# Optimization experiments

Hardware: AMD Instinct MI355X
Metric: run time of the kernel (lower is better)

Reference implementation:

```python
import jax, jax.numpy as jnp
import numpy as np

H = 128
EPS = 1e-5

def _layernorm(x, g, b):
    mu = jnp.mean(x, axis=-1, keepdims=True)
    var = jnp.mean(jnp.square(x - mu), axis=-1, keepdims=True)
    return (x - mu) * jax.lax.rsqrt(var + EPS) * g + b

def _block(x, W, b, g, be):
    # Linear -> LayerNorm -> ReLU (dropout is identity at eval)
    return jax.nn.relu(_layernorm(x @ W + b, g, be))

def setup_inputs() -> dict:
    key = jax.random.key(0)
    ks = jax.random.split(key, 12)
    B, N, C = 32, 4096, 512
    s1 = 1.0 / np.sqrt(H)
    s2 = 1.0 / np.sqrt(2 * H)
    return {
        "fine_features": jax.random.normal(ks[0], (B, N, H), jnp.float32),
        "coarse_features": jax.random.normal(ks[1], (B, C, H), jnp.float32),
        "global_features": jax.random.normal(ks[2], (B, N, H), jnp.float32),
        "atom_to_coarse": jax.random.randint(ks[3], (B, N), 0, 600),  # some >= C (invalid)
        "W_pool": jax.random.uniform(ks[4], (H, H), jnp.float32, -s1, s1),
        "b_pool": jnp.zeros((H,), jnp.float32),
        "g_pool": jnp.ones((H,), jnp.float32),
        "be_pool": jnp.zeros((H,), jnp.float32),
        "W_unpool": jax.random.uniform(ks[5], (H, H), jnp.float32, -s1, s1),
        "b_unpool": jnp.zeros((H,), jnp.float32),
        "g_unpool": jnp.ones((H,), jnp.float32),
        "be_unpool": jnp.zeros((H,), jnp.float32),
        "W_gate": jax.random.uniform(ks[6], (2 * H, H), jnp.float32, -s2, s2),
        "b_gate": jnp.zeros((H,), jnp.float32),
        "W_glob": jax.random.uniform(ks[7], (2 * H, H), jnp.float32, -s2, s2),
        "b_glob": jnp.zeros((H,), jnp.float32),
        "g_glob": jnp.ones((H,), jnp.float32),
        "be_glob": jnp.zeros((H,), jnp.float32),
    }

def reference(fine_features, coarse_features, global_features, atom_to_coarse,
              W_pool, b_pool, g_pool, be_pool,
              W_unpool, b_unpool, g_unpool, be_unpool,
              W_gate, b_gate, W_glob, b_glob, g_glob, be_glob):
    B, N, Hd = fine_features.shape
    C = coarse_features.shape[1]
    idx = atom_to_coarse
    valid = (idx >= 0) & (idx < C)                      # [B,N]

    # ---- batched scatter-add pooling via flat segment_sum ----
    # invalid atoms routed to extra bucket C per batch element
    seg = jnp.where(valid, idx, C) + jnp.arange(B, dtype=idx.dtype)[:, None] * (C + 1)
    pooled = jax.ops.segment_sum(fine_features.reshape(B * N, Hd),
                                 seg.reshape(-1), num_segments=B * (C + 1))
    pooled = pooled.reshape(B, C + 1, Hd)[:, :C]        # [B,C,H]
    counts = jax.ops.segment_sum(valid.reshape(-1).astype(jnp.float32),
                                 seg.reshape(-1), num_segments=B * (C + 1))
    counts = counts.reshape(B, C + 1)[:, :C]
    coarse_from_fine = pooled / jnp.maximum(counts, 1.0)[..., None]
    coarse_from_fine = _block(coarse_from_fine, W_pool, b_pool, g_pool, be_pool)

    # ---- gather unpooling ----
    safe = jnp.where(valid, idx, 0)
    gathered = jnp.take_along_axis(coarse_features, safe[:, :, None], axis=1)  # [B,N,H]
    fine_from_coarse = jnp.where(valid[..., None], gathered, 0.0)
    fine_from_coarse = _block(fine_from_coarse, W_unpool, b_unpool, g_unpool, be_unpool)

    # ---- gated fusion ----
    fine_gate = jax.nn.sigmoid(jnp.concatenate([fine_features, fine_from_coarse], -1) @ W_gate + b_gate)
    fine_updated = fine_gate * fine_features + (1.0 - fine_gate) * fine_from_coarse
    coarse_gate = jax.nn.sigmoid(jnp.concatenate([coarse_features, coarse_from_fine], -1) @ W_gate + b_gate)
    coarse_updated = coarse_gate * coarse_features + (1.0 - coarse_gate) * coarse_from_fine

    # ---- global injection ----
    fine_wg = _block(jnp.concatenate([fine_updated, global_features], -1), W_glob, b_glob, g_glob, be_glob)
    fine_updated = fine_updated + 0.1 * fine_wg
    glob_c = jnp.broadcast_to(jnp.mean(global_features, axis=1, keepdims=True), (B, C, Hd))
    coarse_wg = _block(jnp.concatenate([coarse_updated, glob_c], -1), W_glob, b_glob, g_glob, be_glob)
    coarse_updated = coarse_updated + 0.1 * coarse_wg
    return (fine_updated, coarse_updated)
```

## Files before the change

### kernel.cpp

```cpp
#include <hip/hip_runtime.h>

typedef __bf16 bf16;
typedef bf16 bf16x8 __attribute__((ext_vector_type(8)));
typedef float f32x4 __attribute__((ext_vector_type(4)));

#define TPM 512
#define UPAD 136

#define NPOOL 1024
#define NGM   512
#define NPREP 64
#define NM1   128
#define NM0   1024

__device__ inline unsigned short f2bf(float f){
  union{ bf16 h; unsigned short u; } v; v.h = (bf16)f; return v.u;
}
__device__ inline float bf2f(unsigned short u){
  union{ unsigned short u; bf16 h; } v; v.u = u; return (float)v.h;
}
__device__ inline unsigned int pk2(float a, float b){
  return (unsigned int)f2bf(a) | ((unsigned int)f2bf(b) << 16);
}
union BF8 { bf16x8 v; unsigned int u[4]; };
__device__ inline bf16x8 pack8(float4 a, float4 b){
  BF8 r; r.u[0] = pk2(a.x, a.y); r.u[1] = pk2(a.z, a.w);
  r.u[2] = pk2(b.x, b.y); r.u[3] = pk2(b.z, b.w); return r.v;
}

__device__ inline void gll16(const unsigned short* g, unsigned short* l){
  __builtin_amdgcn_global_load_lds(
      (const __attribute__((address_space(1))) unsigned int*)g,
      (__attribute__((address_space(3))) unsigned int*)l, 16, 0, 0);
}
__device__ inline void stage_win(const unsigned short* __restrict__ src,
                                 unsigned short* half, int wave, int lane){
#pragma unroll
  for (int i = 0; i < 2; ++i){
    int slice = i*8 + wave;
    gll16(src + slice*512 + lane*8, half + slice*512 + lane*8);
  }
}

__device__ inline void gemm_win(const bf16x8 a[2], const unsigned short* half,
                                f32x4 acc[8], int lane){
#pragma unroll
  for (int kk = 0; kk < 2; ++kk){
    bf16x8 av = a[kk];
#pragma unroll
    for (int n = 0; n < 8; ++n){
      bf16x8 bv = *(const bf16x8*)(half + (size_t)((n*2 + kk)*512) + lane*8);
      acc[n] = __builtin_amdgcn_mfma_f32_16x16x32_bf16(av, bv, acc[n], 0, 0, 0);
    }
  }
}

__device__ inline void rowstats(const f32x4 acc[8], const float bia[8],
                                float mean[4], float rstd[4]){
#pragma unroll
  for (int ri = 0; ri < 4; ++ri){
    float s = 0.f, q = 0.f;
#pragma unroll
    for (int n = 0; n < 8; ++n){
      float z = acc[n][ri] + bia[n];
      s += z; q += z*z;
    }
#pragma unroll
    for (int m = 1; m < 16; m <<= 1){ s += __shfl_xor(s, m); q += __shfl_xor(q, m); }
    mean[ri] = s * (1.f/128.f);
    float var = q * (1.f/128.f) - mean[ri]*mean[ri];
    rstd[ri] = rsqrtf(var + 1e-5f);
  }
}

struct PoolSh {
  int sidx[4096];
  int rows[4096];
  int cnt[16], off[17], woff[16];
};
struct GmeanSh { float4 part4[16][32]; };
union PreSh { PoolSh p; GmeanSh g; };

__device__ void pool_body(PoolSh& sh, int pid,
                          const float* __restrict__ fine,
                          const int* __restrict__ idx,
                          unsigned short* __restrict__ pooled){
  int b = pid >> 5, g = pid & 31;
  int c0 = g * 16;
  int tid = threadIdx.x;
  const int* idx_b = idx + b*4096;
#pragma unroll
  for (int i = 0; i < 2; ++i)
    ((int4*)sh.sidx)[tid + i*TPM] = ((const int4*)idx_b)[tid + i*TPM];
  if (tid < 16) sh.cnt[tid] = 0;
  __syncthreads();
  for (int i = tid; i < 4096; i += TPM){
    unsigned d = (unsigned)(sh.sidx[i] - c0);
    if (d < 16u) atomicAdd(&sh.cnt[d], 1);
  }
  __syncthreads();
  if (tid == 0){
    int s = 0;
#pragma unroll
    for (int j = 0; j < 16; ++j){ sh.off[j] = s; s += sh.cnt[j]; }
    sh.off[16] = s;
  }
  __syncthreads();
  if (tid < 16) sh.woff[tid] = sh.off[tid];
  __syncthreads();
  for (int i = tid; i < 4096; i += TPM){
    unsigned d = (unsigned)(sh.sidx[i] - c0);
    if (d < 16u){ int p = atomicAdd(&sh.woff[d], 1); sh.rows[p] = i; }
  }
  __syncthreads();
  int hw = tid >> 5, l32 = tid & 31;
  const float* fb = fine + (size_t)b*4096*128;
  int o0 = sh.off[hw], o1 = sh.off[hw+1];
  float4 s = {0.f, 0.f, 0.f, 0.f};
  int m = o0;
  for (; m + 3 < o1; m += 4){
    float4 v0 = *((const float4*)(fb + (size_t)sh.rows[m+0]*128) + l32);
    float4 v1 = *((const float4*)(fb + (size_t)sh.rows[m+1]*128) + l32);
    float4 v2 = *((const float4*)(fb + (size_t)sh.rows[m+2]*128) + l32);
    float4 v3 = *((const float4*)(fb + (size_t)sh.rows[m+3]*128) + l32);
    s.x += (v0.x + v1.x) + (v2.x + v3.x);
    s.y += (v0.y + v1.y) + (v2.y + v3.y);
    s.z += (v0.z + v1.z) + (v2.z + v3.z);
    s.w += (v0.w + v1.w) + (v2.w + v3.w);
  }
  for (; m < o1; ++m){
    float4 v = *((const float4*)(fb + (size_t)sh.rows[m]*128) + l32);
    s.x += v.x; s.y += v.y; s.z += v.z; s.w += v.w;
  }
  float inv = 1.f / fmaxf((float)(o1 - o0), 1.f);
  unsigned short* po = pooled + ((size_t)(b*512 + c0 + hw))*128 + l32*4;
  uint2 w2; w2.x = pk2(s.x*inv, s.y*inv); w2.y = pk2(s.z*inv, s.w*inv);
  *(uint2*)po = w2;
}

__device__ void gmean_body(GmeanSh& sh, int gid,
                           const float* __restrict__ glob,
                           float* __restrict__ gmean){
  int b = gid >> 4, ch = gid & 15;
  int tid = threadIdx.x;
  int c4 = tid & 31, rg = tid >> 5;
  const float* gb = glob + ((size_t)b*4096 + ch*256)*128;
  float4 a = {0.f, 0.f, 0.f, 0.f};
#pragma unroll
  for (int i = 0; i < 16; ++i){
    int r = rg + i*16;
    float4 v = *(const float4*)(gb + (size_t)r*128 + c4*4);
    a.x += v.x; a.y += v.y; a.z += v.z; a.w += v.w;
  }
  sh.part4[rg][c4] = a;
  __syncthreads();
  if (tid < 32){
    float4 s = sh.part4[0][tid];
#pragma unroll
    for (int g = 1; g < 16; ++g){
      float4 v = sh.part4[g][tid];
      s.x += v.x; s.y += v.y; s.z += v.z; s.w += v.w;
    }
    float* gm = gmean + b*128 + tid*4;
    atomicAdd(&gm[0], s.x); atomicAdd(&gm[1], s.y);
    atomicAdd(&gm[2], s.z); atomicAdd(&gm[3], s.w);
  }
}

__device__ void prep_body(int e,
                          const float* __restrict__ Wp, const float* __restrict__ Wu,
                          const float* __restrict__ Wg, const float* __restrict__ Wgl,
                          unsigned short* __restrict__ WfP, unsigned short* __restrict__ WfU,
                          unsigned short* __restrict__ WfG, unsigned short* __restrict__ WfGl){
  int j = e & 7, lane = (e >> 3) & 63, frag = e >> 9;
  int kk = frag & 1, nblk = (frag >> 1) & 7, c = frag >> 4;
  int il = lane & 15, lg = lane >> 4;
  int col = nblk*16 + il;
  int k = c*64 + kk*32 + lg*8 + j;
  if (e < 16384){
    WfP[e] = f2bf(Wp[k*128 + col]);
    WfU[e] = f2bf(Wu[k*128 + col]);
  }
  WfG[e]  = f2bf(Wg[k*128 + col]);
  WfGl[e] = f2bf(Wgl[k*128 + col]);
}

__global__ __launch_bounds__(TPM) void k_pre(
    const float* __restrict__ fine, const int* __restrict__ idx,
    const float* __restrict__ glob,
    const float* __restrict__ Wp, const float* __restrict__ Wu,
    const float* __restrict__ Wg, const float* __restrict__ Wgl,
    unsigned short* __restrict__ pooled, float* __restrict__ gmean,
    unsigned short* __restrict__ WfP, unsigned short* __restrict__ WfU,
    unsigned short* __restrict__ WfG, unsigned short* __restrict__ WfGl){
  __shared__ __align__(16) PreSh sh;
  int bid = blockIdx.x;
  if (bid < NPOOL)             pool_body(sh.p, bid, fine, idx, pooled);
  else if (bid < NPOOL + NGM)  gmean_body(sh.g, bid - NPOOL, glob, gmean);
  else                         prep_body((bid - NPOOL - NGM)*TPM + threadIdx.x,
                                         Wp, Wu, Wg, Wgl, WfP, WfU, WfG, WfGl);
}

struct MegaSh {
  unsigned short wb[2][8192];
  unsigned short ubuf[8][16*UPAD];
};
template<int PATH>
__device__ void mega_body(MegaSh& sh, int bid,
    const float* __restrict__ a_src,
    const float* __restrict__ gath_src,
    const unsigned short* __restrict__ x1b,
    const int* __restrict__ idx,
    const float* __restrict__ gsrc,
    float gscale,
    const unsigned short* __restrict__ Wf1, const float* __restrict__ b1,
    const float* __restrict__ g1, const float* __restrict__ be1,
    const unsigned short* __restrict__ WfG, const float* __restrict__ bG,
    const unsigned short* __restrict__ WfGl, const float* __restrict__ bGl,
    const float* __restrict__ gGl, const float* __restrict__ beGl,
    float* __restrict__ out)
{
  int tid = threadIdx.x;
  int wave = tid >> 6, lane = tid & 63;
  int il = lane & 15, lg = lane >> 4;
  int row0 = bid * 128 + wave * 16;
  int b = (PATH == 0) ? (row0 >> 12) : (row0 >> 9);
  unsigned short* u = sh.ubuf[wave];

  stage_win(Wf1, sh.wb[0], wave, lane);
  bf16x8 a1[4];
  if (PATH == 0){
    int n0 = row0 & 4095;
    int ci = idx[b*4096 + n0 + il];
    bool valid = (unsigned)ci < 512u;
    const float* cr = gath_src + ((size_t)b*512 + (valid ? ci : 0))*128;
#pragma unroll
    for (int c = 0; c < 2; ++c)
#pragma unroll
      for (int kk = 0; kk < 2; ++kk){
        float4 f0 = {0.f,0.f,0.f,0.f}, f1 = {0.f,0.f,0.f,0.f};
        if (valid){
          f0 = *(const float4*)(cr + c*64 + kk*32 + lg*8);
          f1 = *(const float4*)(cr + c*64 + kk*32 + lg*8 + 4);
        }
        a1[c*2 + kk] = pack8(f0, f1);
      }
  } else {
    const unsigned short* pr = x1b + (size_t)(row0 + il)*128;
#pragma unroll
    for (int c = 0; c < 2; ++c)
#pragma unroll
      for (int kk = 0; kk < 2; ++kk)
        a1[c*2 + kk] = *(const bf16x8*)(pr + c*64 + kk*32 + lg*8);
  }
  __syncthreads();

  f32x4 acc[8] = {};
  bf16x8 af[2];
  float4 raw[8];
  const float* ar = a_src + (size_t)(row0 + il)*128;

  stage_win(Wf1 + 8192, sh.wb[1], wave, lane);
  af[0] = a1[0]; af[1] = a1[1];
  gemm_win(af, sh.wb[0], acc, lane);
  __syncthreads();

  stage_win(WfG, sh.wb[0], wave, lane);
  af[0] = a1[2]; af[1] = a1[3];
  gemm_win(af, sh.wb[1], acc, lane);
#pragma unroll
  for (int c = 0; c < 2; ++c)
#pragma unroll
    for (int kk = 0; kk < 2; ++kk){
      raw[(c*2+kk)*2+0] = *(const float4*)(ar + c*64 + kk*32 + lg*8);
      raw[(c*2+kk)*2+1] = *(const float4*)(ar + c*64 + kk*32 + lg*8 + 4);
    }
  {
    float bia[8], gmv[8], btv[8];
#pragma unroll
    for (int n = 0; n < 8; ++n){
      int col = n*16 + il;
      bia[n] = b1[col]; gmv[n] = g1[col]; btv[n] = be1[col];
    }
    float mean[4], rstd[4];
    rowstats(acc, bia, mean, rstd);
#pragma unroll
    for (int ri = 0; ri < 4; ++ri)
#pragma unroll
      for (int n = 0; n < 8; ++n){
        float z = acc[n][ri] + bia[n];
        float y = fmaxf((z - mean[ri])*rstd[ri]*gmv[n] + btv[n], 0.f);
        u[(lg*4 + ri)*UPAD + n*16 + il] = f2bf(y);
      }
  }
  __syncthreads();

  stage_win(WfG + 8192, sh.wb[1], wave, lane);
#pragma unroll
  for (int n = 0; n < 8; ++n) acc[n] = (f32x4){0.f,0.f,0.f,0.f};
  af[0] = pack8(raw[0], raw[1]); af[1] = pack8(raw[2], raw[3]);
  gemm_win(af, sh.wb[0], acc, lane);
  __syncthreads();

  stage_win(WfG + 16384, sh.wb[0], wave, lane);
  af[0] = pack8(raw[4], raw[5]); af[1] = pack8(raw[6], raw[7]);
  gemm_win(af, sh.wb[1], acc, lane);
  __syncthreads();

  stage_win(WfG + 24576, sh.wb[1], wave, lane);
  if (PATH == 0){
    const float* gr = gsrc + (size_t)(row0 + il)*128;
#pragma unroll
    for (int c = 0; c < 2; ++c)
#pragma unroll
      for (int kk = 0; kk < 2; ++kk){
        raw[(c*2+kk)*2+0] = *(const float4*)(gr + c*64 + kk*32 + lg*8);
        raw[(c*2+kk)*2+1] = *(const float4*)(gr + c*64 + kk*32 + lg*8 + 4);
      }
  } else {
    const float* gm = gsrc + b*128;
#pragma unroll
    for (int c = 0; c < 2; ++c)
#pragma unroll
      for (int kk = 0; kk < 2; ++kk){
        float4 f0 = *(const float4*)(gm + c*64 + kk*32 + lg*8);
        float4 f1 = *(const float4*)(gm + c*64 + kk*32 + lg*8 + 4);
        raw[(c*2+kk)*2+0] = (float4){f0.x*gscale, f0.y*gscale, f0.z*gscale, f0.w*gscale};
        raw[(c*2+kk)*2+1] = (float4){f1.x*gscale, f1.y*gscale, f1.z*gscale, f1.w*gscale};
      }
  }
  af[0] = *(const bf16x8*)(u + il*UPAD + 0*64 + 0*32 + lg*8);
  af[1] = *(const bf16x8*)(u + il*UPAD + 0*64 + 1*32 + lg*8);
  gemm_win(af, sh.wb[0], acc, lane);
  __syncthreads();

  stage_win(WfGl, sh.wb[0], wave, lane);
  af[0] = *(const bf16x8*)(u + il*UPAD + 1*64 + 0*32 + lg*8);
  af[1] = *(const bf16x8*)(u + il*UPAD + 1*64 + 1*32 + lg*8);
  gemm_win(af, sh.wb[1], acc, lane);
#pragma unroll
  for (int ri = 0; ri < 4; ++ri){
    int grow = (row0 + lg*4 + ri)*128;
#pragma unroll
    for (int n = 0; n < 8; ++n){
      int col = n*16 + il;
      float z = acc[n][ri] + bG[col];
      float gt = 1.f / (1.f + __expf(-z));
      float f  = a_src[(size_t)grow + col];
      int ua = (lg*4 + ri)*UPAD + col;
      float u1 = bf2f(u[ua]);
      u[ua] = f2bf(gt*f + (1.f - gt)*u1);
    }
  }
  __syncthreads();

  stage_win(WfGl + 8192, sh.wb[1], wave, lane);
#pragma unroll
  for (int n = 0; n < 8; ++n) acc[n] = (f32x4){0.f,0.f,0.f,0.f};
  af[0] = *(const bf16x8*)(u + il*UPAD + 0*64 + 0*32 + lg*8);
  af[1] = *(const bf16x8*)(u + il*UPAD + 0*64 + 1*32 + lg*8);
  gemm_win(af, sh.wb[0], acc, lane);
  __syncthreads();

  stage_win(WfGl + 16384, sh.wb[0], wave, lane);
  af[0] = *(const bf16x8*)(u + il*UPAD + 1*64 + 0*32 + lg*8);
  af[1] = *(const bf16x8*)(u + il*UPAD + 1*64 + 1*32 + lg*8);
  gemm_win(af, sh.wb[1], acc, lane);
  __syncthreads();

  stage_win(WfGl + 24576, sh.wb[1], wave, lane);
  af[0] = pack8(raw[0], raw[1]); af[1] = pack8(raw[2], raw[3]);
  gemm_win(af, sh.wb[0], acc, lane);
  __syncthreads();

  af[0] = pack8(raw[4], raw[5]); af[1] = pack8(raw[6], raw[7]);
  gemm_win(af, sh.wb[1], acc, lane);
  {
    float bia[8], gmv[8], btv[8];
#pragma unroll
    for (int n = 0; n < 8; ++n){
      int col = n*16 + il;
      bia[n] = bGl[col]; gmv[n] = gGl[col]; btv[n] = beGl[col];
    }
    float mean[4], rstd[4];
    rowstats(acc, bia, mean, rstd);
#pragma unroll
    for (int ri = 0; ri < 4; ++ri){
      int grow = (row0 + lg*4 + ri)*128;
#pragma unroll
      for (int n = 0; n < 8; ++n){
        int col = n*16 + il;
        float z = acc[n][ri] + bia[n];
        float y = fmaxf((z - mean[ri])*rstd[ri]*gmv[n] + btv[n], 0.f);
        float u2 = bf2f(u[(lg*4 + ri)*UPAD + col]);
        out[(size_t)grow + col] = u2 + 0.1f*y;
      }
    }
  }
}

__global__ __launch_bounds__(TPM, 4) void k_mega(
    const float* __restrict__ fine,
    const float* __restrict__ coarse,
    const int* __restrict__ idx,
    const float* __restrict__ glob,
    const unsigned short* __restrict__ pooled,
    const float* __restrict__ gmean,
    const unsigned short* __restrict__ WfP, const float* __restrict__ bP,
    const float* __restrict__ gP, const float* __restrict__ beP,
    const unsigned short* __restrict__ WfU, const float* __restrict__ bU,
    const float* __restrict__ gU, const float* __restrict__ beU,
    const unsigned short* __restrict__ WfG, const float* __restrict__ bG,
    const unsigned short* __restrict__ WfGl, const float* __restrict__ bGl,
    const float* __restrict__ gGl, const float* __restrict__ beGl,
    float* __restrict__ out_fine,
    float* __restrict__ out_coarse)
{
  __shared__ __align__(16) MegaSh sh;
  int bid = blockIdx.x;
  if (bid < NM1){
    mega_body<1>(sh, bid, coarse, nullptr, pooled, nullptr, gmean, 1.f/4096.f,
                 WfP, bP, gP, beP, WfG, bG, WfGl, bGl, gGl, beGl, out_coarse);
  } else {
    mega_body<0>(sh, bid - NM1, fine, coarse, nullptr, idx, glob, 1.0f,
                 WfU, bU, gU, beU, WfG, bG, WfGl, bGl, gGl, beGl, out_fine);
  }
}

extern "C" void kernel_launch(void* const* d_in, const int* in_sizes, int n_in,
                              void* d_out, int out_size, void* d_ws, size_t ws_size,
                              hipStream_t stream){
  const float* fine    = (const float*)d_in[0];
  const float* coarse  = (const float*)d_in[1];
  const float* glob    = (const float*)d_in[2];
  const int*   idx     = (const int*)  d_in[3];
  const float* W_pool  = (const float*)d_in[4];
  const float* b_pool  = (const float*)d_in[5];
  const float* g_pool  = (const float*)d_in[6];
  const float* be_pool = (const float*)d_in[7];
  const float* W_unpool  = (const float*)d_in[8];
  const float* b_unpool  = (const float*)d_in[9];
  const float* g_unpool  = (const float*)d_in[10];
  const float* be_unpool = (const float*)d_in[11];
  const float* W_gate = (const float*)d_in[12];
  const float* b_gate = (const float*)d_in[13];
  const float* W_glob = (const float*)d_in[14];
  const float* b_glob = (const float*)d_in[15];
  const float* g_glob = (const float*)d_in[16];
  const float* be_glob= (const float*)d_in[17];

  const int B = 32, N = 4096, C = 512;
  float* out_fine   = (float*)d_out;
  float* out_coarse = out_fine + (size_t)B*N*128;

  char* w = (char*)d_ws;
  unsigned short* WfP  = (unsigned short*)w; w += 16384*2;
  unsigned short* WfU  = (unsigned short*)w; w += 16384*2;
  unsigned short* WfG  = (unsigned short*)w; w += 32768*2;
  unsigned short* WfGl = (unsigned short*)w; w += 32768*2;
  float* gmean = (float*)w;                  w += B*128*4;
  unsigned short* pooled = (unsigned short*)w; w += (size_t)B*C*128*2;

  hipMemsetAsync(gmean, 0, B*128*4, stream);
  k_pre<<<NPOOL + NGM + NPREP, TPM, 0, stream>>>(
      fine, idx, glob, W_pool, W_unpool, W_gate, W_glob,
      pooled, gmean, WfP, WfU, WfG, WfGl);

  k_mega<<<NM1 + NM0, TPM, 0, stream>>>(
      fine, coarse, idx, glob, pooled, gmean,
      WfP, b_pool, g_pool, be_pool,
      WfU, b_unpool, g_unpool, be_unpool,
      WfG, b_gate, WfGl, b_glob, g_glob, be_glob,
      out_fine, out_coarse);
}
```

Measured before the change: 106.6 us.

## Halve mega-kernel block size and stream weights in finer 32-K double-buffered slices

Splits the mega kernel into 256-thread blocks covering 64 rows, doubling the grid, and separates the pool kernel's thread count from it. Weights are restaged in 8 KB slices, one per 32-wide K step, across a single 20-step double-buffered loop instead of 16 KB windows. The prep kernel's fragment layout is reordered to match. This halves LDS per block to allow more resident blocks and finer overlap of loads with MFMA, at the cost of more __syncthreads and weights being reloaded by twice as many blocks.

Result: slower. 262.9 us (+146.6%).

```diff
diff --git a/kernel.cpp b/kernel.cpp
--- a/kernel.cpp
+++ b/kernel.cpp
@@ -4,14 +4,15 @@
 typedef bf16 bf16x8 __attribute__((ext_vector_type(8)));
 typedef float f32x4 __attribute__((ext_vector_type(4)));
 
-#define TPM 512
+#define TPP 512
+#define TPM 256
 #define UPAD 136
 
 #define NPOOL 1024
 #define NGM   512
 #define NPREP 64
-#define NM1   128
-#define NM0   1024
+#define NM1   256
+#define NM0   2048
 
 __device__ inline unsigned short f2bf(float f){
   union{ bf16 h; unsigned short u; } v; v.h = (bf16)f; return v.u;
@@ -33,25 +34,18 @@
       (const __attribute__((address_space(1))) unsigned int*)g,
       (__attribute__((address_space(3))) unsigned int*)l, 16, 0, 0);
 }
-__device__ inline void stage_win(const unsigned short* __restrict__ src,
-                                 unsigned short* half, int wave, int lane){
-#pragma unroll
-  for (int i = 0; i < 2; ++i){
-    int slice = i*8 + wave;
-    gll16(src + slice*512 + lane*8, half + slice*512 + lane*8);
-  }
-}
-
-__device__ inline void gemm_win(const bf16x8 a[2], const unsigned short* half,
-                                f32x4 acc[8], int lane){
-#pragma unroll
-  for (int kk = 0; kk < 2; ++kk){
-    bf16x8 av = a[kk];
-#pragma unroll
-    for (int n = 0; n < 8; ++n){
-      bf16x8 bv = *(const bf16x8*)(half + (size_t)((n*2 + kk)*512) + lane*8);
-      acc[n] = __builtin_amdgcn_mfma_f32_16x16x32_bf16(av, bv, acc[n], 0, 0, 0);
-    }
+__device__ inline void stage8(const unsigned short* __restrict__ src,
+                              unsigned short* dst, int tid){
+  gll16(src + tid*8, dst + tid*8);
+  gll16(src + (tid + TPM)*8, dst + (tid + TPM)*8);
+}
+
+__device__ inline void gemm8(bf16x8 av, const unsigned short* wbuf,
+                             f32x4 acc[8], int lane){
+#pragma unroll
+  for (int n = 0; n < 8; ++n){
+    bf16x8 bv = *(const bf16x8*)(wbuf + n*512 + lane*8);
+    acc[n] = __builtin_amdgcn_mfma_f32_16x16x32_bf16(av, bv, acc[n], 0, 0, 0);
   }
 }
 
@@ -91,10 +85,10 @@
   const int* idx_b = idx + b*4096;
 #pragma unroll
   for (int i = 0; i < 2; ++i)
-    ((int4*)sh.sidx)[tid + i*TPM] = ((const int4*)idx_b)[tid + i*TPM];
+    ((int4*)sh.sidx)[tid + i*TPP] = ((const int4*)idx_b)[tid + i*TPP];
   if (tid < 16) sh.cnt[tid] = 0;
   __syncthreads();
-  for (int i = tid; i < 4096; i += TPM){
+  for (int i = tid; i < 4096; i += TPP){
     unsigned d = (unsigned)(sh.sidx[i] - c0);
     if (d < 16u) atomicAdd(&sh.cnt[d], 1);
   }
@@ -108,7 +102,7 @@
   __syncthreads();
   if (tid < 16) sh.woff[tid] = sh.off[tid];
   __syncthreads();
-  for (int i = tid; i < 4096; i += TPM){
+  for (int i = tid; i < 4096; i += TPP){
     unsigned d = (unsigned)(sh.sidx[i] - c0);
     if (d < 16u){ int p = atomicAdd(&sh.woff[d], 1); sh.rows[p] = i; }
   }
@@ -173,9 +167,10 @@
                           unsigned short* __restrict__ WfP, unsigned short* __restrict__ WfU,
                           unsigned short* __restrict__ WfG, unsigned short* __restrict__ WfGl){
   int j = e & 7, lane = (e >> 3) & 63, frag = e >> 9;
-  int kk = frag & 1, nblk = (frag >> 1) & 7, c = frag >> 4;
+  int n = frag & 7, kkc = frag >> 3;
+  int kk = kkc & 1, c = kkc >> 1;
   int il = lane & 15, lg = lane >> 4;
-  int col = nblk*16 + il;
+  int col = n*16 + il;
   int k = c*64 + kk*32 + lg*8 + j;
   if (e < 16384){
     WfP[e] = f2bf(Wp[k*128 + col]);
@@ -185,7 +180,7 @@
   WfGl[e] = f2bf(Wgl[k*128 + col]);
 }
 
-__global__ __launch_bounds__(TPM) void k_pre(
+__global__ __launch_bounds__(TPP) void k_pre(
     const float* __restrict__ fine, const int* __restrict__ idx,
     const float* __restrict__ glob,
     const float* __restrict__ Wp, const float* __restrict__ Wu,
@@ -197,13 +192,13 @@
   int bid = blockIdx.x;
   if (bid < NPOOL)             pool_body(sh.p, bid, fine, idx, pooled);
   else if (bid < NPOOL + NGM)  gmean_body(sh.g, bid - NPOOL, glob, gmean);
-  else                         prep_body((bid - NPOOL - NGM)*TPM + threadIdx.x,
+  else                         prep_body((bid - NPOOL - NGM)*TPP + threadIdx.x,
                                          Wp, Wu, Wg, Wgl, WfP, WfU, WfG, WfGl);
 }
 
 struct MegaSh {
-  unsigned short wb[2][8192];
-  unsigned short ubuf[8][16*UPAD];
+  unsigned short wb[2][4096];
+  unsigned short ubuf[4][16*UPAD];
 };
 template<int PATH>
 __device__ void mega_body(MegaSh& sh, int bid,
@@ -223,11 +218,11 @@
   int tid = threadIdx.x;
   int wave = tid >> 6, lane = tid & 63;
   int il = lane & 15, lg = lane >> 4;
-  int row0 = bid * 128 + wave * 16;
+  int row0 = bid * 64 + wave * 16;
   int b = (PATH == 0) ? (row0 >> 12) : (row0 >> 9);
   unsigned short* u = sh.ubuf[wave];
 
-  stage_win(Wf1, sh.wb[0], wave, lane);
+  stage8(Wf1, sh.wb[0], tid);
   bf16x8 a1[4];
   if (PATH == 0){
     int n0 = row0 & 4095;
@@ -256,146 +251,120 @@
   __syncthreads();
 
   f32x4 acc[8] = {};
-  bf16x8 af[2];
   float4 raw[8];
   const float* ar = a_src + (size_t)(row0 + il)*128;
 
-  stage_win(Wf1 + 8192, sh.wb[1], wave, lane);
-  af[0] = a1[0]; af[1] = a1[1];
-  gemm_win(af, sh.wb[0], acc, lane);
-  __syncthreads();
-
-  stage_win(WfG, sh.wb[0], wave, lane);
-  af[0] = a1[2]; af[1] = a1[3];
-  gemm_win(af, sh.wb[1], acc, lane);
-#pragma unroll
-  for (int c = 0; c < 2; ++c)
-#pragma unroll
-    for (int kk = 0; kk < 2; ++kk){
-      raw[(c*2+kk)*2+0] = *(const float4*)(ar + c*64 + kk*32 + lg*8);
-      raw[(c*2+kk)*2+1] = *(const float4*)(ar + c*64 + kk*32 + lg*8 + 4);
-    }
-  {
-    float bia[8], gmv[8], btv[8];
-#pragma unroll
-    for (int n = 0; n < 8; ++n){
-      int col = n*16 + il;
-      bia[n] = b1[col]; gmv[n] = g1[col]; btv[n] = be1[col];
-    }
-    float mean[4], rstd[4];
-    rowstats(acc, bia, mean, rstd);
-#pragma unroll
-    for (int ri = 0; ri < 4; ++ri)
-#pragma unroll
-      for (int n = 0; n < 8; ++n){
-        float z = acc[n][ri] + bia[n];
-        float y = fmaxf((z - mean[ri])*rstd[ri]*gmv[n] + btv[n], 0.f);
-        u[(lg*4 + ri)*UPAD + n*16 + il] = f2bf(y);
-      }
-  }
-  __syncthreads();
-
-  stage_win(WfG + 8192, sh.wb[1], wave, lane);
-#pragma unroll
-  for (int n = 0; n < 8; ++n) acc[n] = (f32x4){0.f,0.f,0.f,0.f};
-  af[0] = pack8(raw[0], raw[1]); af[1] = pack8(raw[2], raw[3]);
-  gemm_win(af, sh.wb[0], acc, lane);
-  __syncthreads();
-
-  stage_win(WfG + 16384, sh.wb[0], wave, lane);
-  af[0] = pack8(raw[4], raw[5]); af[1] = pack8(raw[6], raw[7]);
-  gemm_win(af, sh.wb[1], acc, lane);
-  __syncthreads();
-
-  stage_win(WfG + 24576, sh.wb[1], wave, lane);
-  if (PATH == 0){
-    const float* gr = gsrc + (size_t)(row0 + il)*128;
-#pragma unroll
-    for (int c = 0; c < 2; ++c)
-#pragma unroll
-      for (int kk = 0; kk < 2; ++kk){
-        raw[(c*2+kk)*2+0] = *(const float4*)(gr + c*64 + kk*32 + lg*8);
-        raw[(c*2+kk)*2+1] = *(const float4*)(gr + c*64 + kk*32 + lg*8 + 4);
-      }
-  } else {
-    const float* gm = gsrc + b*128;
-#pragma unroll
-    for (int c = 0; c < 2; ++c)
-#pragma unroll
-      for (int kk = 0; kk < 2; ++kk){
-        float4 f0 = *(const float4*)(gm + c*64 + kk*32 + lg*8);
-        float4 f1 = *(const float4*)(gm + c*64 + kk*32 + lg*8 + 4);
-        raw[(c*2+kk)*2+0] = (float4){f0.x*gscale, f0.y*gscale, f0.z*gscale, f0.w*gscale};
-        raw[(c*2+kk)*2+1] = (float4){f1.x*gscale, f1.y*gscale, f1.z*gscale, f1.w*gscale};
-      }
-  }
-  af[0] = *(const bf16x8*)(u + il*UPAD + 0*64 + 0*32 + lg*8);
-  af[1] = *(const bf16x8*)(u + il*UPAD + 0*64 + 1*32 + lg*8);
-  gemm_win(af, sh.wb[0], acc, lane);
-  __syncthreads();
-
-  stage_win(WfGl, sh.wb[0], wave, lane);
-  af[0] = *(const bf16x8*)(u + il*UPAD + 1*64 + 0*32 + lg*8);
-  af[1] = *(const bf16x8*)(u + il*UPAD + 1*64 + 1*32 + lg*8);
-  gemm_win(af, sh.wb[1], acc, lane);
-#pragma unroll
-  for (int ri = 0; ri < 4; ++ri){
-    int grow = (row0 + lg*4 + ri)*128;
-#pragma unroll
-    for (int n = 0; n < 8; ++n){
-      int col = n*16 + il;
-      float z = acc[n][ri] + bG[col];
-      float gt = 1.f / (1.f + __expf(-z));
-      float f  = a_src[(size_t)grow + col];
-      int ua = (lg*4 + ri)*UPAD + col;
-      float u1 = bf2f(u[ua]);
-      u[ua] = f2bf(gt*f + (1.f - gt)*u1);
-    }
-  }
-  __syncthreads();
-
-  stage_win(WfGl + 8192, sh.wb[1], wave, lane);
-#pragma unroll
-  for (int n = 0; n < 8; ++n) acc[n] = (f32x4){0.f,0.f,0.f,0.f};
-  af[0] = *(const bf16x8*)(u + il*UPAD + 0*64 + 0*32 + lg*8);
-  af[1] = *(const bf16x8*)(u + il*UPAD + 0*64 + 1*32 + lg*8);
-  gemm_win(af, sh.wb[0], acc, lane);
-  __syncthreads();
-
-  stage_win(WfGl + 16384, sh.wb[0], wave, lane);
-  af[0] = *(const bf16x8*)(u + il*UPAD + 1*64 + 0*32 + lg*8);
-  af[1] = *(const bf16x8*)(u + il*UPAD + 1*64 + 1*32 + lg*8);
-  gemm_win(af, sh.wb[1], acc, lane);
-  __syncthreads();
-
-  stage_win(WfGl + 24576, sh.wb[1], wave, lane);
-  af[0] = pack8(raw[0], raw[1]); af[1] = pack8(raw[2], raw[3]);
-  gemm_win(af, sh.wb[0], acc, lane);
-  __syncthreads();
-
-  af[0] = pack8(raw[4], raw[5]); af[1] = pack8(raw[6], raw[7]);
-  gemm_win(af, sh.wb[1], acc, lane);
-  {
-    float bia[8], gmv[8], btv[8];
-#pragma unroll
-    for (int n = 0; n < 8; ++n){
-      int col = n*16 + il;
-      bia[n] = bGl[col]; gmv[n] = gGl[col]; btv[n] = beGl[col];
-    }
-    float mean[4], rstd[4];
-    rowstats(acc, bia, mean, rstd);
-#pragma unroll
-    for (int ri = 0; ri < 4; ++ri){
-      int grow = (row0 + lg*4 + ri)*128;
+#pragma unroll
+  for (int p = 0; p < 20; ++p){
+    if (p < 19){
+      int q = p + 1;
+      const unsigned short* ws;
+      if (q < 4)       ws = Wf1  + q*4096;
+      else if (q < 12) ws = WfG  + (q-4)*4096;
+      else             ws = WfGl + (q-12)*4096;
+      stage8(ws, sh.wb[q & 1], tid);
+    }
+    if (p == 4 || p == 12){
+#pragma unroll
+      for (int n = 0; n < 8; ++n) acc[n] = (f32x4){0.f,0.f,0.f,0.f};
+    }
+    bf16x8 av;
+    if (p < 4)        av = a1[p];
+    else if (p < 8){  int l = p-4;  av = pack8(raw[2*l], raw[2*l+1]); }
+    else if (p < 12){ int l = p-8;  av = *(const bf16x8*)(u + il*UPAD + (l>>1)*64 + (l&1)*32 + lg*8); }
+    else if (p < 16){ int l = p-12; av = *(const bf16x8*)(u + il*UPAD + (l>>1)*64 + (l&1)*32 + lg*8); }
+    else {            int l = p-16; av = pack8(raw[2*l], raw[2*l+1]); }
+    gemm8(av, sh.wb[p & 1], acc, lane);
+
+    if (p == 1){
+#pragma unroll
+      for (int c = 0; c < 2; ++c)
+#pragma unroll
+        for (int kk = 0; kk < 2; ++kk){
+          raw[(c*2+kk)*2+0] = *(const float4*)(ar + c*64 + kk*32 + lg*8);
+          raw[(c*2+kk)*2+1] = *(const float4*)(ar + c*64 + kk*32 + lg*8 + 4);
+        }
+    }
+    if (p == 3){
+      float bia[8], gmv[8], btv[8];
 #pragma unroll
       for (int n = 0; n < 8; ++n){
         int col = n*16 + il;
-        float z = acc[n][ri] + bia[n];
-        float y = fmaxf((z - mean[ri])*rstd[ri]*gmv[n] + btv[n], 0.f);
-        float u2 = bf2f(u[(lg*4 + ri)*UPAD + col]);
-        out[(size_t)grow + col] = u2 + 0.1f*y;
-      }
-    }
+        bia[n] = b1[col]; gmv[n] = g1[col]; btv[n] = be1[col];
+      }
+      float mean[4], rstd[4];
+      rowstats(acc, bia, mean, rstd);
+#pragma unroll
+      for (int ri = 0; ri < 4; ++ri)
+#pragma unroll
+        for (int n = 0; n < 8; ++n){
+          float z = acc[n][ri] + bia[n];
+          float y = fmaxf((z - mean[ri])*rstd[ri]*gmv[n] + btv[n], 0.f);
+          u[(lg*4 + ri)*UPAD + n*16 + il] = f2bf(y);
+        }
+    }
+    if (p == 7){
+      if (PATH == 0){
+        const float* gr = gsrc + (size_t)(row0 + il)*128;
+#pragma unroll
+        for (int c = 0; c < 2; ++c)
+#pragma unroll
+          for (int kk = 0; kk < 2; ++kk){
+            raw[(c*2+kk)*2+0] = *(const float4*)(gr + c*64 + kk*32 + lg*8);
+            raw[(c*2+kk)*2+1] = *(const float4*)(gr + c*64 + kk*32 + lg*8 + 4);
+          }
+      } else {
+        const float* gm = gsrc + b*128;
+#pragma unroll
+        for (int c = 0; c < 2; ++c)
+#pragma unroll
+          for (int kk = 0; kk < 2; ++kk){
+            float4 f0 = *(const float4*)(gm + c*64 + kk*32 + lg*8);
+            float4 f1 = *(const float4*)(gm + c*64 + kk*32 + lg*8 + 4);
+            raw[(c*2+kk)*2+0] = (float4){f0.x*gscale, f0.y*gscale, f0.z*gscale, f0.w*gscale};
+            raw[(c*2+kk)*2+1] = (float4){f1.x*gscale, f1.y*gscale, f1.z*gscale, f1.w*gscale};
+          }
+      }
+    }
+    if (p == 11){
+#pragma unroll
+      for (int ri = 0; ri < 4; ++ri){
+        int grow = (row0 + lg*4 + ri)*128;
+#pragma unroll
+        for (int n = 0; n < 8; ++n){
+          int col = n*16 + il;
+          float z = acc[n][ri] + bG[col];
+          float gt = 1.f / (1.f + __expf(-z));
+          float f  = a_src[(size_t)grow + col];
+          int ua = (lg*4 + ri)*UPAD + col;
+          float u1 = bf2f(u[ua]);
+          u[ua] = f2bf(gt*f + (1.f - gt)*u1);
+        }
+      }
+    }
+    if (p == 19){
+      float bia[8], gmv[8], btv[8];
+#pragma unroll
+      for (int n = 0; n < 8; ++n){
+        int col = n*16 + il;
+        bia[n] = bGl[col]; gmv[n] = gGl[col]; btv[n] = beGl[col];
+      }
+      float mean[4], rstd[4];
+      rowstats(acc, bia, mean, rstd);
+#pragma unroll
+      for (int ri = 0; ri < 4; ++ri){
+        int grow = (row0 + lg*4 + ri)*128;
+#pragma unroll
+        for (int n = 0; n < 8; ++n){
+          int col = n*16 + il;
+          float z = acc[n][ri] + bia[n];
+          float y = fmaxf((z - mean[ri])*rstd[ri]*gmv[n] + btv[n], 0.f);
+          float u2 = bf2f(u[(lg*4 + ri)*UPAD + col]);
+          out[(size_t)grow + col] = u2 + 0.1f*y;
+        }
+      }
+    }
+    if (p < 19) __syncthreads();
   }
 }
 
@@ -462,7 +431,7 @@
   unsigned short* pooled = (unsigned short*)w; w += (size_t)B*C*128*2;
 
   hipMemsetAsync(gmean, 0, B*128*4, stream);
-  k_pre<<<NPOOL + NGM + NPREP, TPM, 0, stream>>>(
+  k_pre<<<NPOOL + NGM + NPREP, TPP, 0, stream>>>(
       fine, idx, glob, W_pool, W_unpool, W_gate, W_glob,
       pooled, gmean, WfP, WfU, WfG, WfGl);
 
```
